# Optimization experiments

Hardware: AMD Instinct MI355X
Metric: run time of the kernel (lower is better)

Reference implementation:

```python
import jax, jax.numpy as jnp
import numpy as np

B, N, E, D = 8, 2048, 4096, 256
HOPS = 3

def setup_inputs() -> dict:
    key = jax.random.key(0)
    ks = jax.random.split(key, 12)
    p = lambda k, shp: (jax.random.normal(k, shp, dtype=jnp.float32) * 0.02)
    return {
        "node_vec": jax.random.normal(ks[0], (B, N, D), dtype=jnp.float32),
        "edge_vec": jax.random.normal(ks[1], (B, E, D), dtype=jnp.float32),
        "node2edge": jax.random.uniform(ks[2], (B, E, N), dtype=jnp.float32),
        "edge2node": jax.random.uniform(ks[3], (B, N, E), dtype=jnp.float32),
        "node_mask": jnp.ones((B, N), dtype=jnp.float32),
        "W_fuse": p(ks[4], (D, 2 * D)), "b_fuse": jnp.zeros((D,), jnp.float32),
        "W_z": p(ks[5], (D, 4 * D)), "b_z": jnp.zeros((D,), jnp.float32),
        "W_update": p(ks[6], (D, 2 * D)),
        "W_reset": p(ks[7], (D, 2 * D)),
        "W_memory": p(ks[8], (D, 2 * D)),
        "W_max": p(ks[9], (D, D)),
    }

def _gnn_step(node_vec, edge_vec, n2e, e2n, W_fuse, b_fuse):
    # n2e: [B,E,N], e2n: [B,N,E]
    edge_emb = jnp.einsum('ben,bnd->bed', n2e, node_vec)          # [B,E,D]
    edge_emb = jax.nn.relu(jnp.concatenate([edge_emb, edge_vec], axis=-1) @ W_fuse.T + b_fuse)
    norm = jnp.sum(e2n, axis=2, keepdims=True) + 1.0               # [B,N,1]
    return (jnp.einsum('bne,bed->bnd', e2n, edge_emb) + node_vec) / norm

def _gated_fusion(in_vec, out_vec, W_z, b_z):
    feats = jnp.concatenate([in_vec, out_vec, in_vec * out_vec, in_vec - out_vec], axis=-1)
    z = jax.nn.sigmoid(feats @ W_z.T + b_z)
    return (1.0 - z) * in_vec + z * out_vec

def _gru_step(cur, new, W_u, W_r, W_m):
    cn = jnp.concatenate([cur, new], axis=-1)
    u = jax.nn.sigmoid(cn @ W_u.T)
    r = jax.nn.sigmoid(cn @ W_r.T)
    m = jnp.tanh(jnp.concatenate([r * cur, new], axis=-1) @ W_m.T)
    return (1.0 - u) * cur + u * m

def reference(node_vec, edge_vec, node2edge, edge2node, node_mask,
              W_fuse, b_fuse, W_z, b_z, W_update, W_reset, W_memory, W_max):
    n2e_T = jnp.swapaxes(node2edge, 1, 2)  # [B,N,E]
    e2n_T = jnp.swapaxes(edge2node, 1, 2)  # [B,E,N]
    for _ in range(HOPS):
        out_vec = _gnn_step(node_vec, edge_vec, node2edge, edge2node, W_fuse, b_fuse)
        in_vec = _gnn_step(node_vec, edge_vec, e2n_T, n2e_T, W_fuse, b_fuse)
        new_vec = _gated_fusion(in_vec, out_vec, W_z, b_z)
        node_vec = _gru_step(node_vec, new_vec, W_update, W_reset, W_memory)
    # graph max-pooling: linear then max over nodes (node_mask unused, as in original)
    graph_embedding = jnp.max(node_vec @ W_max.T, axis=1)          # [B,D]
    return (jnp.swapaxes(node_vec, 0, 1), graph_embedding[None])    # [N,B,D], [1,B,D]
```

## Files before the change

kernel.cpp:

```cpp
#include <hip/hip_runtime.h>
#include <math.h>

#define Bb 8
#define Nn 2048
#define Ee 4096
#define Dd 256
#define HOPS 3

typedef __attribute__((ext_vector_type(4))) float f32x4;
typedef _Float16 f16;
typedef __attribute__((ext_vector_type(8))) _Float16 f16x8;
typedef __attribute__((ext_vector_type(4))) _Float16 f16x4;
typedef __attribute__((ext_vector_type(8))) short s16x8;
typedef __attribute__((ext_vector_type(4))) short s16x4;

__device__ __forceinline__ short f2bf(float f){
  union{float f; unsigned u;} x; x.f=f;
  unsigned r = (x.u + 0x7fffu + ((x.u>>16)&1u)) >> 16;
  return (short)r;
}
__device__ __forceinline__ float bf2f(short h){
  union{unsigned u; float f;} x; x.u = ((unsigned)(unsigned short)h) << 16; return x.f;
}
__device__ __forceinline__ int swz(int row, int idx){ return idx ^ ((row & 7) << 3); }

enum { HN=0, HT=1 };
enum { OF=0, OH=1, OHT=2 };
enum { EP_NONE=0, EP_BIAS, EP_ADDRELU, EP_AGG };
enum { SM_CN=0, SM_G4, SM_RC };
enum { SE_GATE=0, SE_SIG, SE_TANH };

template<int AMODE, bool AH, int SPL, int EPI, int OUTM>
__global__ __launch_bounds__(512) void hgemm(
    const void* __restrict__ Av, const f16* __restrict__ Bh, void* __restrict__ Cv,
    const float* __restrict__ aux1, const float* __restrict__ aux2,
    const float* __restrict__ bias,
    int M, int Nd, int K, int lda, int ldb, int ldc,
    long sA, long sB, long sC, long sAux1, long sAux2,
    long aLo, long bLo, int maskB, int mask1)
{
  const int bz = blockIdx.z;
  const char* Ab = (const char*)Av + (AH ? bz * sA * 2 : bz * sA * 4);
  Bh += (long)(bz & maskB) * sB;
  char* Cb = (char*)Cv + ((OUTM == OF) ? bz * sC * 4 : bz * sC * 2);
  if (aux1) aux1 += (long)(bz & mask1) * sAux1;
  if (aux2) aux2 += bz * sAux2;
  const int m0 = blockIdx.y * 128;
  const int n0 = blockIdx.x * 128;

  constexpr int HLA = 128 * 64;
  constexpr int HLB = 128 * 64;
  __shared__ f16 As[128 * 64 * ((SPL & 2) ? 2 : 1)];
  __shared__ f16 Bs[128 * 64 * ((SPL & 1) ? 2 : 1)];

  const int tid = threadIdx.x;
  const int wid = tid >> 6, lane = tid & 63;
  const int wm = (wid >> 1) * 32, wn = (wid & 1) * 64;
  const int r = lane & 15, g = lane >> 4;

  f32x4 acc[2][4];
  #pragma unroll
  for (int i = 0; i < 2; i++)
    #pragma unroll
    for (int j = 0; j < 4; j++) acc[i][j] = (f32x4){0.f, 0.f, 0.f, 0.f};

  f16x8 ra0, ra1, rl0, rl1;
  f16x8 rb0, rb1, rbl0, rbl1;

  auto loadA = [&](int k0) {
    if (AMODE == HN && AH) {
      const f16* Ah = (const f16*)Ab;
      const int row = tid >> 2, kc = (tid & 3) * 16;
      const long off = (long)(m0 + row) * lda + k0 + kc;
      ra0 = *(const f16x8*)&Ah[off];
      ra1 = *(const f16x8*)&Ah[off + 8];
      if (SPL & 2) { rl0 = *(const f16x8*)&Ah[aLo + off]; rl1 = *(const f16x8*)&Ah[aLo + off + 8]; }
    } else if (AMODE == HN && !AH) {
      const float* Af = (const float*)Ab;
      const int row = tid >> 2, kc = (tid & 3) * 16;
      const float* s = &Af[(long)(m0 + row) * lda + k0 + kc];
      f32x4 v0 = *(const f32x4*)s,       v1 = *(const f32x4*)(s + 4);
      f32x4 v2 = *(const f32x4*)(s + 8), v3 = *(const f32x4*)(s + 12);
      ra0 = (f16x8){(f16)v0.x,(f16)v0.y,(f16)v0.z,(f16)v0.w,(f16)v1.x,(f16)v1.y,(f16)v1.z,(f16)v1.w};
      ra1 = (f16x8){(f16)v2.x,(f16)v2.y,(f16)v2.z,(f16)v2.w,(f16)v3.x,(f16)v3.y,(f16)v3.z,(f16)v3.w};
    } else {
      const int mm = tid & 127, kh = (tid >> 7) * 16;
      if (AH) {
        const f16* s = &((const f16*)Ab)[(long)(k0 + kh) * lda + m0 + mm];
        #pragma unroll
        for (int j = 0; j < 8; j++) ra0[j] = s[(long)j * lda];
        #pragma unroll
        for (int j = 0; j < 8; j++) ra1[j] = s[(long)(j + 8) * lda];
      } else {
        const float* s = &((const float*)Ab)[(long)(k0 + kh) * lda + m0 + mm];
        #pragma unroll
        for (int j = 0; j < 8; j++) ra0[j] = (f16)s[(long)j * lda];
        #pragma unroll
        for (int j = 0; j < 8; j++) ra1[j] = (f16)s[(long)(j + 8) * lda];
      }
    }
  };
  auto storeA = [&]() {
    if (AMODE == HT) {
      const int mm = tid & 127, kh = (tid >> 7) * 16;
      *(f16x8*)&As[swz(mm, mm * 64 + kh)]     = ra0;
      *(f16x8*)&As[swz(mm, mm * 64 + kh + 8)] = ra1;
    } else {
      const int row = tid >> 2, kc = (tid & 3) * 16;
      const int i0 = swz(row, row * 64 + kc), i1 = swz(row, row * 64 + kc + 8);
      *(f16x8*)&As[i0] = ra0;
      *(f16x8*)&As[i1] = ra1;
      if (SPL & 2) { *(f16x8*)&As[HLA + i0] = rl0; *(f16x8*)&As[HLA + i1] = rl1; }
    }
  };
  auto loadB = [&](int k0) {
    const int row = tid >> 2, kc = (tid & 3) * 16;
    const long off = (long)(n0 + row) * ldb + k0 + kc;
    rb0 = *(const f16x8*)&Bh[off];
    rb1 = *(const f16x8*)&Bh[off + 8];
    if (SPL & 1) { rbl0 = *(const f16x8*)&Bh[bLo + off]; rbl1 = *(const f16x8*)&Bh[bLo + off + 8]; }
  };
  auto storeB = [&]() {
    const int row = tid >> 2, kc = (tid & 3) * 16;
    const int i0 = swz(row, row * 64 + kc), i1 = swz(row, row * 64 + kc + 8);
    *(f16x8*)&Bs[i0] = rb0;
    *(f16x8*)&Bs[i1] = rb1;
    if (SPL & 1) { *(f16x8*)&Bs[HLB + i0] = rbl0; *(f16x8*)&Bs[HLB + i1] = rbl1; }
  };

  loadA(0); loadB(0);
  storeA(); storeB();
  __syncthreads();

  const int NT = K >> 6;
  for (int t = 0; t < NT; t++) {
    const bool more = (t + 1 < NT);
    if (more) { loadA((t + 1) << 6); loadB((t + 1) << 6); }
    #pragma unroll
    for (int ks = 0; ks < 2; ks++) {
      f16x8 af[2], bf[4], afl[2], bfl[4];
      #pragma unroll
      for (int i = 0; i < 2; i++) {
        const int rw = wm + i * 16 + r;
        const int ix = swz(rw, rw * 64 + ks * 32 + g * 8);
        af[i] = *(const f16x8*)&As[ix];
        if (SPL & 2) afl[i] = *(const f16x8*)&As[HLA + ix];
      }
      #pragma unroll
      for (int j = 0; j < 4; j++) {
        const int rw = wn + j * 16 + r;
        const int ix = swz(rw, rw * 64 + ks * 32 + g * 8);
        bf[j] = *(const f16x8*)&Bs[ix];
        if (SPL & 1) bfl[j] = *(const f16x8*)&Bs[HLB + ix];
      }
      #pragma unroll
      for (int i = 0; i < 2; i++)
        #pragma unroll
        for (int j = 0; j < 4; j++) {
          acc[i][j] = __builtin_amdgcn_mfma_f32_16x16x32_f16(af[i], bf[j], acc[i][j], 0, 0, 0);
          if (SPL & 1)
            acc[i][j] = __builtin_amdgcn_mfma_f32_16x16x32_f16(af[i], bfl[j], acc[i][j], 0, 0, 0);
          if (SPL & 2)
            acc[i][j] = __builtin_amdgcn_mfma_f32_16x16x32_f16(afl[i], bf[j], acc[i][j], 0, 0, 0);
        }
    }
    __syncthreads();
    if (more) { storeA(); storeB(); __syncthreads(); }
  }

  if (OUTM == OHT) {
    f16* tile = (f16*)Bs;
    #pragma unroll
    for (int half = 0; half < 2; half++) {
      __syncthreads();
      if ((wm >> 6) == half) {
        #pragma unroll
        for (int i = 0; i < 2; i++)
          #pragma unroll
          for (int j = 0; j < 4; j++) {
            const int rowl = wm + i * 16 + g * 4 - 64 * half;
            const int coll = wn + j * 16 + r;
            #pragma unroll
            for (int t = 0; t < 4; t++) {
              float v = acc[i][j][t];
              if (EPI == EP_ADDRELU) {
                v += aux1[(long)(m0 + 64 * half + rowl + t) * 256 + n0 + coll];
                v = v > 0.f ? v : 0.f;
              } else if (EPI == EP_BIAS) { v += bias[n0 + coll]; }
              tile[coll * 72 + rowl + t] = (f16)v;
            }
          }
      }
      __syncthreads();
      const int c2 = tid >> 2, rs = (tid & 3) * 16;
      f16* dst = &((f16*)Cb)[(long)(n0 + c2) * ldc + m0 + 64 * half + rs];
      *(f16x8*)dst       = *(const f16x8*)&tile[c2 * 72 + rs];
      *(f16x8*)(dst + 8) = *(const f16x8*)&tile[c2 * 72 + rs + 8];
    }
  } else {
    #pragma unroll
    for (int i = 0; i < 2; i++) {
      #pragma unroll
      for (int j = 0; j < 4; j++) {
        const int rowb = m0 + wm + i * 16 + g * 4;
        const int col = n0 + wn + j * 16 + r;
        #pragma unroll
        for (int t = 0; t < 4; t++) {
          const int row = rowb + t;
          const long idx = (long)row * ldc + col;
          float v = acc[i][j][t];
          if (EPI == EP_BIAS)         { v += bias[col]; }
          else if (EPI == EP_ADDRELU) { v += aux1[(long)row * 256 + col]; v = v > 0.f ? v : 0.f; }
          else if (EPI == EP_AGG)     { v = (v + aux1[idx]) * aux2[row]; }
          if (OUTM == OH) ((f16*)Cb)[idx] = (f16)v;
          else            ((float*)Cb)[idx] = v;
        }
      }
    }
  }
}

template<int AMODE, int EPI>
__global__ __launch_bounds__(512) void ggemm(
    const float* __restrict__ A, const float* __restrict__ A2, const float* __restrict__ A3,
    const short* __restrict__ Bw, float* __restrict__ C,
    const float* __restrict__ aux1, const float* __restrict__ aux2, const float* __restrict__ bias,
    int Nd, int K, int lda, int ldb, int ldc, long bLo)
{
  const int m0 = blockIdx.y * 128;
  const int n0 = blockIdx.x * 128;
  constexpr int HLA = 128 * 64;
  constexpr int HLB = 128 * 64;
  __shared__ short As[128 * 64 * 2];
  __shared__ short Bs[128 * 64 * 2];

  const int tid = threadIdx.x;
  const int wid = tid >> 6, lane = tid & 63;
  const int wm = (wid >> 1) * 32, wn = (wid & 1) * 64;
  const int r = lane & 15, g = lane >> 4;

  f32x4 acc[2][4];
  #pragma unroll
  for (int i = 0; i < 2; i++)
    #pragma unroll
    for (int j = 0; j < 4; j++) acc[i][j] = (f32x4){0.f, 0.f, 0.f, 0.f};

  s16x4 rah[4], ral[4];
  s16x8 rbh0, rbh1, rbl0, rbl1;

  auto loadA = [&](int k0) {
    const int row = tid >> 2, kc = (tid & 3) * 16;
    const int kk = k0 + kc, q = kk >> 8, kd = kk & 255;
    const long base = (long)(m0 + row) * 256 + kd;
    const long baseA = (long)(m0 + row) * lda + kd;
    #pragma unroll
    for (int u = 0; u < 4; u++) {
      f32x4 v;
      if (AMODE == SM_CN) {
        v = (q == 0) ? *(const f32x4*)(A + base + 4 * u)
                     : *(const f32x4*)(A2 + base + 4 * u);
      } else if (AMODE == SM_G4) {
        if (q == 0)      v = *(const f32x4*)(A  + base + 4 * u);
        else if (q == 1) v = *(const f32x4*)(A2 + base + 4 * u);
        else {
          f32x4 x = *(const f32x4*)(A  + base + 4 * u);
          f32x4 y = *(const f32x4*)(A2 + base + 4 * u);
          v = (q == 2) ? x * y : x - y;
        }
      } else {
        if (q == 0) {
          f32x4 x = *(const f32x4*)(A  + baseA + 4 * u);
          f32x4 y = *(const f32x4*)(A2 + base + 4 * u);
          v = x * y;
        } else v = *(const f32x4*)(A3 + base + 4 * u);
      }
      s16x4 h = { f2bf(v.x), f2bf(v.y), f2bf(v.z), f2bf(v.w) };
      rah[u] = h;
      ral[u] = (s16x4){ f2bf(v.x - bf2f(h.x)), f2bf(v.y - bf2f(h.y)),
                        f2bf(v.z - bf2f(h.z)), f2bf(v.w - bf2f(h.w)) };
    }
  };
  auto storeA = [&]() {
    const int row = tid >> 2, kc = (tid & 3) * 16;
    const int i0 = swz(row, row * 64 + kc), i1 = swz(row, row * 64 + kc + 8);
    *(s16x4*)&As[i0]     = rah[0]; *(s16x4*)&As[i0 + 4] = rah[1];
    *(s16x4*)&As[i1]     = rah[2]; *(s16x4*)&As[i1 + 4] = rah[3];
    *(s16x4*)&As[HLA + i0]     = ral[0]; *(s16x4*)&As[HLA + i0 + 4] = ral[1];
    *(s16x4*)&As[HLA + i1]     = ral[2]; *(s16x4*)&As[HLA + i1 + 4] = ral[3];
  };
  auto loadB = [&](int k0) {
    const int row = tid >> 2, kc = (tid & 3) * 16;
    const long off = (long)(n0 + row) * ldb + k0 + kc;
    rbh0 = *(const s16x8*)&Bw[off];
    rbh1 = *(const s16x8*)&Bw[off + 8];
    rbl0 = *(const s16x8*)&Bw[bLo + off];
    rbl1 = *(const s16x8*)&Bw[bLo + off + 8];
  };
  auto storeB = [&]() {
    const int row = tid >> 2, kc = (tid & 3) * 16;
    const int i0 = swz(row, row * 64 + kc), i1 = swz(row, row * 64 + kc + 8);
    *(s16x8*)&Bs[i0] = rbh0;
    *(s16x8*)&Bs[i1] = rbh1;
    *(s16x8*)&Bs[HLB + i0] = rbl0;
    *(s16x8*)&Bs[HLB + i1] = rbl1;
  };

  loadA(0); loadB(0);
  storeA(); storeB();
  __syncthreads();

  const int NT = K >> 6;
  for (int t = 0; t < NT; t++) {
    const bool more = (t + 1 < NT);
    if (more) { loadA((t + 1) << 6); loadB((t + 1) << 6); }
    #pragma unroll
    for (int ks = 0; ks < 2; ks++) {
      s16x8 ah[2], al[2], bh[4], bl[4];
      #pragma unroll
      for (int i = 0; i < 2; i++) {
        const int rw = wm + i * 16 + r;
        const int ix = swz(rw, rw * 64 + ks * 32 + g * 8);
        ah[i] = *(const s16x8*)&As[ix];
        al[i] = *(const s16x8*)&As[HLA + ix];
      }
      #pragma unroll
      for (int j = 0; j < 4; j++) {
        const int rw = wn + j * 16 + r;
        const int ix = swz(rw, rw * 64 + ks * 32 + g * 8);
        bh[j] = *(const s16x8*)&Bs[ix];
        bl[j] = *(const s16x8*)&Bs[HLB + ix];
      }
      #pragma unroll
      for (int i = 0; i < 2; i++)
        #pragma unroll
        for (int j = 0; j < 4; j++) {
          acc[i][j] = __builtin_amdgcn_mfma_f32_16x16x32_bf16(ah[i], bh[j], acc[i][j], 0, 0, 0);
          acc[i][j] = __builtin_amdgcn_mfma_f32_16x16x32_bf16(ah[i], bl[j], acc[i][j], 0, 0, 0);
          acc[i][j] = __builtin_amdgcn_mfma_f32_16x16x32_bf16(al[i], bh[j], acc[i][j], 0, 0, 0);
        }
    }
    __syncthreads();
    if (more) { storeA(); storeB(); __syncthreads(); }
  }

  #pragma unroll
  for (int i = 0; i < 2; i++) {
    #pragma unroll
    for (int j = 0; j < 4; j++) {
      #pragma unroll
      for (int t = 0; t < 4; t++) {
        const int row = m0 + wm + i * 16 + g * 4 + t;
        const int col = n0 + wn + j * 16 + r;
        float v = acc[i][j][t];
        if (EPI == SE_GATE) {
          v += bias[col];
          float z = 1.f / (1.f + __expf(-v));
          const long ix = (long)row * 256 + col;
          v = (1.f - z) * aux1[ix] + z * aux2[ix];
        } else if (EPI == SE_SIG) {
          v = 1.f / (1.f + __expf(-v));
        } else {
          v = tanhf(v);
        }
        C[(long)row * ldc + col] = v;
      }
    }
  }
}


__global__ void cvt_n2e_colsum(const float* __restrict__ n2e, f16* __restrict__ n2e_h,
                               float* __restrict__ part) {
  const int n = blockIdx.x * 256 + threadIdx.x;
  const int c = blockIdx.y, b = blockIdx.z;
  const long base = (long)b * Ee * Nn + (long)c * 256 * Nn + n;
  float s = 0.f;
  for (int e = 0; e < 256; e++) {
    float v = n2e[base + (long)e * Nn];
    n2e_h[base + (long)e * Nn] = (f16)v;
    s += v;
  }
  part[((long)b * 16 + c) * Nn + n] = s;
}

__global__ void cvt_e2n_rowsum(const float* __restrict__ e2n, f16* __restrict__ e2n_h,
                               float* __restrict__ rno) {
  const long row = blockIdx.x;
  const int tid = threadIdx.x, lane = tid & 63, wid = tid >> 6;
  const float* p = e2n + row * Ee;
  f16* ph = e2n_h + row * Ee;
  float s = 0.f;
  for (int e = tid; e < Ee; e += 256) { float v = p[e]; ph[e] = (f16)v; s += v; }
  #pragma unroll
  for (int off = 32; off; off >>= 1) s += __shfl_down(s, off);
  __shared__ float wsum[4];
  if (lane == 0) wsum[wid] = s;
  __syncthreads();
  if (tid == 0) rno[row] = 1.f / (1.f + wsum[0] + wsum[1] + wsum[2] + wsum[3]);
}

__global__ void adjT(const f16* __restrict__ in, f16* __restrict__ out, int R, int C) {
  __shared__ f16 t[64][72];
  const long boff = (long)blockIdx.z * R * C;
  const int r0 = blockIdx.x * 64, c0 = blockIdx.y * 64;
  const int tid = threadIdx.x;
  const int rl = tid >> 2, cl = (tid & 3) * 16;
  const f16* src = in + boff + (long)(r0 + rl) * C + c0 + cl;
  *(f16x8*)&t[rl][cl]     = *(const f16x8*)src;
  *(f16x8*)&t[rl][cl + 8] = *(const f16x8*)(src + 8);
  __syncthreads();
  const int cl2 = tid >> 2, rl2 = (tid & 3) * 16;
  f16x8 o0, o1;
  #pragma unroll
  for (int v = 0; v < 8; v++) { o0[v] = t[rl2 + v][cl2]; o1[v] = t[rl2 + 8 + v][cl2]; }
  f16* dst = out + boff + (long)(c0 + cl2) * R + r0 + rl2;
  *(f16x8*)dst = o0;
  *(f16x8*)(dst + 8) = o1;
}

__global__ void rowsum_kernel(const float* __restrict__ e2n, float* __restrict__ out) {
  const int gw = blockIdx.x * 4 + (threadIdx.x >> 6);
  const int lane = threadIdx.x & 63;
  const float* p = e2n + (long)gw * Ee;
  float s = 0.f;
  for (int e = lane; e < Ee; e += 64) s += p[e];
  #pragma unroll
  for (int off = 32; off; off >>= 1) s += __shfl_down(s, off);
  if (lane == 0) out[gw] = 1.f / (1.f + s);
}
__global__ void colsum_kernel(const float* __restrict__ n2e, float* __restrict__ part) {
  const int n = blockIdx.x * 256 + threadIdx.x;
  const int c = blockIdx.y, b = blockIdx.z;
  const float* p = n2e + (long)b * Ee * Nn + (long)c * 256 * Nn + n;
  float s = 0.f;
  for (int e = 0; e < 256; e++) s += p[(long)e * Nn];
  part[((long)b * 16 + c) * Nn + n] = s;
}
__global__ void colfin_kernel(const float* __restrict__ part, float* __restrict__ rni) {
  const int i = blockIdx.x * 256 + threadIdx.x;
  const int b = i >> 11, n = i & 2047;
  float s = 0.f;
  #pragma unroll
  for (int c = 0; c < 16; c++) s += part[((long)b * 16 + c) * Nn + n];
  rni[i] = 1.f / (1.f + s);
}

__global__ void cvt_half(const float* __restrict__ src, f16* __restrict__ dst) {
  const long i4 = (long)blockIdx.x * 256 + threadIdx.x;
  f32x4 v = *(const f32x4*)&src[i4 * 4];
  *(f16x4*)&dst[i4 * 4] = (f16x4){(f16)v.x, (f16)v.y, (f16)v.z, (f16)v.w};
}

__global__ void cvt_half_split(const float* __restrict__ src, f16* __restrict__ dst, long loOff) {
  const long i4 = (long)blockIdx.x * 256 + threadIdx.x;
  f32x4 v = *(const f32x4*)&src[i4 * 4];
  f16x4 h = {(f16)v.x, (f16)v.y, (f16)v.z, (f16)v.w};
  *(f16x4*)&dst[i4 * 4] = h;
  f16x4 l = {(f16)(v.x - (float)h[0]), (f16)(v.y - (float)h[1]),
             (f16)(v.z - (float)h[2]), (f16)(v.w - (float)h[3])};
  *(f16x4*)&dst[loOff + i4 * 4] = l;
}

__global__ void cvt_bf_split(const float* __restrict__ src, short* __restrict__ dst, long loOff) {
  const long i4 = (long)blockIdx.x * 256 + threadIdx.x;
  f32x4 v = *(const f32x4*)&src[i4 * 4];
  s16x4 h = { f2bf(v.x), f2bf(v.y), f2bf(v.z), f2bf(v.w) };
  *(s16x4*)&dst[i4 * 4] = h;
  s16x4 l = { f2bf(v.x - bf2f(h.x)), f2bf(v.y - bf2f(h.y)),
              f2bf(v.z - bf2f(h.z)), f2bf(v.w - bf2f(h.w)) };
  *(s16x4*)&dst[loOff + i4 * 4] = l;
}

__global__ void init_cur(const float* __restrict__ node_vec, float* __restrict__ cur,
                         f16* __restrict__ cur_h, long loOff) {
  const long i4 = (long)blockIdx.x * 256 + threadIdx.x;
  f32x4 v = *(const f32x4*)&node_vec[i4 * 4];
  *(f32x4*)&cur[i4 * 4] = v;
  f16x4 h = {(f16)v.x, (f16)v.y, (f16)v.z, (f16)v.w};
  *(f16x4*)&cur_h[i4 * 4] = h;
  f16x4 l = {(f16)(v.x - (float)h[0]), (f16)(v.y - (float)h[1]),
             (f16)(v.z - (float)h[2]), (f16)(v.w - (float)h[3])};
  *(f16x4*)&cur_h[loOff + i4 * 4] = l;
}

__global__ void transposeT(const float* __restrict__ cur, f16* __restrict__ curT, long loOff) {
  __shared__ f16 th[64][72];
  __shared__ f16 tl[64][72];
  const int b = blockIdx.z, nt = blockIdx.x * 64, dt = blockIdx.y * 64;
  const int tid = threadIdx.x;
  const int nl = tid >> 2, d0 = (tid & 3) * 16;
  const float* src = cur + ((long)b * Nn + nt + nl) * 256 + dt + d0;
  #pragma unroll
  for (int u = 0; u < 4; u++) {
    f32x4 v = *(const f32x4*)(src + 4 * u);
    f16x4 h = {(f16)v.x, (f16)v.y, (f16)v.z, (f16)v.w};
    *(f16x4*)&th[nl][d0 + 4 * u] = h;
    f16x4 l = {(f16)(v.x - (float)h[0]), (f16)(v.y - (float)h[1]),
               (f16)(v.z - (float)h[2]), (f16)(v.w - (float)h[3])};
    *(f16x4*)&tl[nl][d0 + 4 * u] = l;
  }
  __syncthreads();
  const int dl = tid >> 2, n0l = (tid & 3) * 16;
  f16x8 o0, o1, p0, p1;
  #pragma unroll
  for (int v = 0; v < 8; v++) {
    o0[v] = th[n0l + v][dl];     o1[v] = th[n0l + 8 + v][dl];
    p0[v] = tl[n0l + v][dl];     p1[v] = tl[n0l + 8 + v][dl];
  }
  f16* dst = curT + (long)b * (256 * Nn) + (long)(dt + dl) * Nn + nt + n0l;
  *(f16x8*)dst = o0;
  *(f16x8*)(dst + 8) = o1;
  *(f16x8*)(dst + loOff) = p0;
  *(f16x8*)(dst + loOff + 8) = p1;
}

__global__ void gruf_kernel(const float* __restrict__ urb, const float* __restrict__ m,
                            float* __restrict__ cur, f16* __restrict__ cur_h, long loOff) {
  const long i = (long)blockIdx.x * 256 + threadIdx.x;
  const long bn = i >> 8; const int d = i & 255;
  const float uu = urb[bn * 512 + d];
  const float v = (1.f - uu) * cur[i] + uu * m[i];
  cur[i] = v;
  f16 h = (f16)v;
  cur_h[i] = h;
  cur_h[loOff + i] = (f16)(v - (float)h);
}

__global__ void maxpool1(const float* __restrict__ pooled, float* __restrict__ part) {
  const int d = threadIdx.x, c = blockIdx.x, b = blockIdx.y;
  const float* p = pooled + ((long)b * Nn + c * 256) * Dd + d;
  float m = -INFINITY;
  for (int n = 0; n < 256; n++) m = fmaxf(m, p[(long)n * Dd]);
  part[(b * 8 + c) * Dd + d] = m;
}
__global__ void maxpool2(const float* __restrict__ part, float* __restrict__ out1) {
  const int d = threadIdx.x, b = blockIdx.x;
  float m = -INFINITY;
  #pragma unroll
  for (int c = 0; c < 8; c++) m = fmaxf(m, part[(b * 8 + c) * Dd + d]);
  out1[b * Dd + d] = m;
}
__global__ void transpose_out(const float* __restrict__ cur, float* __restrict__ out0) {
  const long i = (long)blockIdx.x * 256 + threadIdx.x;
  const int d = i & 255;
  const long nb = i >> 8;
  const int b = nb & 7;
  const long n = nb >> 3;
  out0[i] = cur[((long)b * Nn + n) * Dd + d];
}

extern "C" void kernel_launch(void* const* d_in, const int* in_sizes, int n_in,
                              void* d_out, int out_size, void* d_ws, size_t ws_size,
                              hipStream_t stream) {
  const float* node_vec = (const float*)d_in[0];
  const float* edge_vec = (const float*)d_in[1];
  const float* n2e      = (const float*)d_in[2];
  const float* e2n      = (const float*)d_in[3];
  const float* W_fuse   = (const float*)d_in[5];
  const float* b_fuse   = (const float*)d_in[6];
  const float* W_z      = (const float*)d_in[7];
  const float* b_z      = (const float*)d_in[8];
  const float* W_u      = (const float*)d_in[9];
  const float* W_r      = (const float*)d_in[10];
  const float* W_m      = (const float*)d_in[11];
  const float* W_max    = (const float*)d_in[12];

  const long ND  = (long)Bb * Nn * Dd;
  const long EDb = (long)Ee * Dd;
  const long NDb = (long)Nn * Dd;
  const long ED  = (long)Bb * EDb;
  const long ADJb = (long)Ee * Nn;
  const long ADJ = (long)Bb * ADJb;
  const int  BN  = Bb * Nn;

  char* p = (char*)d_ws;
  auto alloc = [&](size_t bytes) { char* r = p; p += (bytes + 255) & ~(size_t)255; return r; };

  const size_t need_full =
      (size_t)4 * ADJ * 2
      + (size_t)ED * 2
      + (size_t)4 * ED * 2
      + (size_t)ED * 4
      + (size_t)4 * ND * 2
      + (size_t)(2 * 131072 + 2 * 65536) * 2
      + (size_t)(2 * 262144 + 2 * 262144 + 2 * 131072) * 2
      + (size_t)5 * ND * 4
      + (size_t)BN * 512 * 4
      + (size_t)(2 * BN + 16 * BN + BN) * 4
      + 64 * 1024;
  const bool full = ws_size >= need_full;

  f16 *adjEO = nullptr, *adjAG = nullptr;
  f16 *n2e_h = nullptr, *e2n_hT = nullptr, *e2n_h = nullptr, *n2e_hT = nullptr;
  if (full) {
    adjEO = (f16*)alloc((size_t)2 * ADJ * 2);
    adjAG = (f16*)alloc((size_t)2 * ADJ * 2);
    n2e_h = adjEO;  e2n_hT = adjEO + ADJ;
    e2n_h = adjAG;  n2e_hT = adjAG + ADJ;
  }
  f16* ev_h    = (f16*)alloc(ED * 2);
  f16* E1h2    = (f16*)alloc((size_t)2 * ED * 2);
  f16* E2T2    = (f16*)alloc((size_t)2 * ED * 2);
  float* EVW   = (float*)alloc(ED * 4);
  f16* cur_h   = (f16*)alloc(2 * ND * 2);
  f16* cur_hT  = (f16*)alloc(2 * ND * 2);
  f16* Wf_h    = (f16*)alloc(2 * 131072 * 2);
  f16* Wmax_h  = (f16*)alloc(2 * 65536 * 2);
  short* Wz_s  = (short*)alloc((size_t)2 * 262144 * 2);
  short* Wur_s = (short*)alloc((size_t)2 * 262144 * 2);
  short* Wm_s  = (short*)alloc((size_t)2 * 131072 * 2);
  float* cur   = (float*)alloc(ND * 4);
  float* outv  = (float*)alloc(2 * ND * 4);
  float* inv   = outv + ND;
  float* nv    = (float*)alloc(ND * 4);
  float* urb   = (float*)alloc((size_t)BN * 512 * 4);
  float* mb    = (float*)alloc(ND * 4);
  float* rno   = (float*)alloc(2 * BN * 4);
  float* rni   = rno + BN;
  float* colpart = (float*)alloc((size_t)16 * BN * 4);
  float* maxpart = (float*)alloc(BN * 4);

  float* out0 = (float*)d_out;
  float* out1 = out0 + ND;

  if (full) {
    cvt_n2e_colsum<<<dim3(Nn / 256, 16, Bb), 256, 0, stream>>>(n2e, n2e_h, colpart);
    colfin_kernel<<<BN / 256, 256, 0, stream>>>(colpart, rni);
    cvt_e2n_rowsum<<<BN, 256, 0, stream>>>(e2n, e2n_h, rno);
    adjT<<<dim3(Ee / 64, Nn / 64, Bb), 256, 0, stream>>>(n2e_h, n2e_hT, Ee, Nn);
    adjT<<<dim3(Nn / 64, Ee / 64, Bb), 256, 0, stream>>>(e2n_h, e2n_hT, Nn, Ee);
  } else {
    colsum_kernel<<<dim3(Nn / 256, 16, Bb), 256, 0, stream>>>(n2e, colpart);
    colfin_kernel<<<BN / 256, 256, 0, stream>>>(colpart, rni);
    rowsum_kernel<<<BN / 4, 256, 0, stream>>>(e2n, rno);
  }
  cvt_half<<<(int)(ED / 1024), 256, 0, stream>>>(edge_vec, ev_h);
  cvt_half_split<<<131072 / 1024, 256, 0, stream>>>(W_fuse, Wf_h, 131072);
  cvt_half_split<<<65536 / 1024, 256, 0, stream>>>(W_max, Wmax_h, 65536);
  cvt_bf_split<<<262144 / 1024, 256, 0, stream>>>(W_z, Wz_s, 262144);
  cvt_bf_split<<<131072 / 1024, 256, 0, stream>>>(W_u, Wur_s, 262144);
  cvt_bf_split<<<131072 / 1024, 256, 0, stream>>>(W_r, Wur_s + 131072, 262144);
  cvt_bf_split<<<131072 / 1024, 256, 0, stream>>>(W_m, Wm_s, 131072);
  init_cur<<<(int)(ND / 1024), 256, 0, stream>>>(node_vec, cur, cur_h, ND);
  transposeT<<<dim3(Nn / 64, 4, Bb), 256, 0, stream>>>(cur, cur_hT, ND);

  hgemm<HN, true, 1, EP_BIAS, OF><<<dim3(2, Ee / 128, Bb), 512, 0, stream>>>(
      ev_h, Wf_h + 256, EVW, nullptr, nullptr, b_fuse,
      Ee, 256, 256, 256, 512, 256, EDb, 0, EDb, 0, 0, 0, 131072, 0, 0);

  for (int h = 0; h < HOPS; h++) {
    if (full) {
      hgemm<HN, true, 1, EP_NONE, OH><<<dim3(2, Ee / 128, 2 * Bb), 512, 0, stream>>>(
          adjEO, cur_hT, E1h2, nullptr, nullptr, nullptr,
          Ee, 256, Nn, Nn, Nn, 256, ADJb, NDb, EDb, 0, 0, 0, ND, 7, 0);
      hgemm<HN, true, 1, EP_ADDRELU, OHT><<<dim3(2, Ee / 128, 2 * Bb), 512, 0, stream>>>(
          E1h2, Wf_h, E2T2, EVW, nullptr, nullptr,
          Ee, 256, 256, 256, 512, Ee, EDb, 0, EDb, EDb, 0, 0, 131072, 0, 7);
      hgemm<HN, true, 0, EP_AGG, OF><<<dim3(2, Nn / 128, 2 * Bb), 512, 0, stream>>>(
          adjAG, E2T2, outv, cur, rno, nullptr,
          Nn, 256, Ee, Ee, Ee, 256, ADJb, EDb, NDb, NDb, (long)Nn, 0, 0, 15, 7);
    } else {
      hgemm<HN, false, 1, EP_NONE, OH><<<dim3(2, Ee / 128, Bb), 512, 0, stream>>>(
          n2e, cur_hT, E1h2, nullptr, nullptr, nullptr,
          Ee, 256, Nn, Nn, Nn, 256, ADJb, NDb, EDb, 0, 0, 0, ND, 7, 0);
      hgemm<HT, false, 1, EP_NONE, OH><<<dim3(2, Ee / 128, Bb), 512, 0, stream>>>(
          e2n, cur_hT, E1h2 + ED, nullptr, nullptr, nullptr,
          Ee, 256, Nn, Ee, Nn, 256, ADJb, NDb, EDb, 0, 0, 0, ND, 7, 0);
      hgemm<HN, true, 1, EP_ADDRELU, OHT><<<dim3(2, Ee / 128, 2 * Bb), 512, 0, stream>>>(
          E1h2, Wf_h, E2T2, EVW, nullptr, nullptr,
          Ee, 256, 256, 256, 512, Ee, EDb, 0, EDb, EDb, 0, 0, 131072, 0, 7);
      hgemm<HN, false, 0, EP_AGG, OF><<<dim3(2, Nn / 128, Bb), 512, 0, stream>>>(
          e2n, E2T2, outv, cur, rno, nullptr,
          Nn, 256, Ee, Ee, Ee, 256, (long)Nn * Ee, EDb, NDb, NDb, (long)Nn, 0, 0, 15, 7);
      hgemm<HT, false, 0, EP_AGG, OF><<<dim3(2, Nn / 128, Bb), 512, 0, stream>>>(
          n2e, E2T2 + ED, inv, cur, rni, nullptr,
          Nn, 256, Ee, Nn, Ee, 256, (long)Ee * Nn, EDb, NDb, NDb, (long)Nn, 0, 0, 15, 7);
    }
    ggemm<SM_G4, SE_GATE><<<dim3(2, BN / 128, 1), 512, 0, stream>>>(
        inv, outv, nullptr, Wz_s, nv, inv, outv, b_z, 256, 1024, 256, 1024, 256, 262144);
    ggemm<SM_CN, SE_SIG><<<dim3(4, BN / 128, 1), 512, 0, stream>>>(
        cur, nv, nullptr, Wur_s, urb, nullptr, nullptr, nullptr, 512, 512, 256, 512, 512, 262144);
    ggemm<SM_RC, SE_TANH><<<dim3(2, BN / 128, 1), 512, 0, stream>>>(
        urb + 256, cur, nv, Wm_s, mb, nullptr, nullptr, nullptr, 256, 512, 512, 512, 256, 131072);
    gruf_kernel<<<(int)(ND / 256), 256, 0, stream>>>(urb, mb, cur, cur_h, ND);
    if (h < HOPS - 1)
      transposeT<<<dim3(Nn / 64, 4, Bb), 256, 0, stream>>>(cur, cur_hT, ND);
  }

  hgemm<HN, true, 3, EP_NONE, OF><<<dim3(2, BN / 128, 1), 512, 0, stream>>>(
      cur_h, Wmax_h, urb, nullptr, nullptr, nullptr,
      BN, 256, 256, 256, 256, 256, 0, 0, 0, 0, 0, ND, 65536, 0, 0);
  maxpool1<<<dim3(8, Bb), 256, 0, stream>>>(urb, maxpart);
  maxpool2<<<Bb, 256, 0, stream>>>(maxpart, out1);

  transpose_out<<<(int)(ND / 256), 256, 0, stream>>>(cur, out0);
}
```

Baseline: 1.709 ms.

## Fuse adjacency fp16 conversion, transpose and sums; store edge projection in fp16

The two-pass preprocessing (convert-plus-sum kernels followed by separate transpose kernels) is replaced by one cvt_dual kernel per adjacency. It reads the fp32 matrix once and writes both the fp16 copy and its transpose, along with partial row or column sums that a small finalize kernel reduces. This removes a full re-read of the fp16 adjacencies. The precomputed edge_vec projection is also stored in fp16 and read as fp16 in the ReLU epilogue, halving that auxiliary traffic at some cost in precision. The sums for the transposed case are now taken from fp16-rounded values.

```diff
diff --git a/kernel.cpp b/kernel.cpp
--- a/kernel.cpp
+++ b/kernel.cpp
@@ -26,7 +26,7 @@
 
 enum { HN=0, HT=1 };
 enum { OF=0, OH=1, OHT=2 };
-enum { EP_NONE=0, EP_BIAS, EP_ADDRELU, EP_AGG };
+enum { EP_NONE=0, EP_BIAS, EP_ADDRELUH, EP_AGG };
 enum { SM_CN=0, SM_G4, SM_RC };
 enum { SE_GATE=0, SE_SIG, SE_TANH };
 
@@ -183,8 +183,8 @@
             #pragma unroll
             for (int t = 0; t < 4; t++) {
               float v = acc[i][j][t];
-              if (EPI == EP_ADDRELU) {
-                v += aux1[(long)(m0 + 64 * half + rowl + t) * 256 + n0 + coll];
+              if (EPI == EP_ADDRELUH) {
+                v += (float)((const f16*)aux1)[(long)(m0 + 64 * half + rowl + t) * 256 + n0 + coll];
                 v = v > 0.f ? v : 0.f;
               } else if (EPI == EP_BIAS) { v += bias[n0 + coll]; }
               tile[coll * 72 + rowl + t] = (f16)v;
@@ -209,9 +209,10 @@
           const int row = rowb + t;
           const long idx = (long)row * ldc + col;
           float v = acc[i][j][t];
-          if (EPI == EP_BIAS)         { v += bias[col]; }
-          else if (EPI == EP_ADDRELU) { v += aux1[(long)row * 256 + col]; v = v > 0.f ? v : 0.f; }
-          else if (EPI == EP_AGG)     { v = (v + aux1[idx]) * aux2[row]; }
+          if (EPI == EP_BIAS)          { v += bias[col]; }
+          else if (EPI == EP_ADDRELUH) { v += (float)((const f16*)aux1)[(long)row * 256 + col];
+                                         v = v > 0.f ? v : 0.f; }
+          else if (EPI == EP_AGG)      { v = (v + aux1[idx]) * aux2[row]; }
           if (OUTM == OH) ((f16*)Cb)[idx] = (f16)v;
           else            ((float*)Cb)[idx] = v;
         }
@@ -369,53 +370,59 @@
 }
 
 
-__global__ void cvt_n2e_colsum(const float* __restrict__ n2e, f16* __restrict__ n2e_h,
-                               float* __restrict__ part) {
-  const int n = blockIdx.x * 256 + threadIdx.x;
-  const int c = blockIdx.y, b = blockIdx.z;
-  const long base = (long)b * Ee * Nn + (long)c * 256 * Nn + n;
-  float s = 0.f;
-  for (int e = 0; e < 256; e++) {
-    float v = n2e[base + (long)e * Nn];
-    n2e_h[base + (long)e * Nn] = (f16)v;
-    s += v;
-  }
-  part[((long)b * 16 + c) * Nn + n] = s;
-}
-
-__global__ void cvt_e2n_rowsum(const float* __restrict__ e2n, f16* __restrict__ e2n_h,
-                               float* __restrict__ rno) {
-  const long row = blockIdx.x;
-  const int tid = threadIdx.x, lane = tid & 63, wid = tid >> 6;
-  const float* p = e2n + row * Ee;
-  f16* ph = e2n_h + row * Ee;
-  float s = 0.f;
-  for (int e = tid; e < Ee; e += 256) { float v = p[e]; ph[e] = (f16)v; s += v; }
-  #pragma unroll
-  for (int off = 32; off; off >>= 1) s += __shfl_down(s, off);
-  __shared__ float wsum[4];
-  if (lane == 0) wsum[wid] = s;
-  __syncthreads();
-  if (tid == 0) rno[row] = 1.f / (1.f + wsum[0] + wsum[1] + wsum[2] + wsum[3]);
-}
-
-__global__ void adjT(const f16* __restrict__ in, f16* __restrict__ out, int R, int C) {
+template<bool SUMDST>
+__global__ void cvt_dual(const float* __restrict__ in, f16* __restrict__ outR,
+                         f16* __restrict__ outT, float* __restrict__ part, int R, int C) {
   __shared__ f16 t[64][72];
-  const long boff = (long)blockIdx.z * R * C;
+  __shared__ float sacc[64][4];
+  const long boff = (long)blockIdx.z * (long)R * C;
   const int r0 = blockIdx.x * 64, c0 = blockIdx.y * 64;
   const int tid = threadIdx.x;
   const int rl = tid >> 2, cl = (tid & 3) * 16;
-  const f16* src = in + boff + (long)(r0 + rl) * C + c0 + cl;
-  *(f16x8*)&t[rl][cl]     = *(const f16x8*)src;
-  *(f16x8*)&t[rl][cl + 8] = *(const f16x8*)(src + 8);
+  const float* src = in + boff + (long)(r0 + rl) * C + c0 + cl;
+  f16 loc[16];
+  float s = 0.f;
+  #pragma unroll
+  for (int u = 0; u < 4; u++) {
+    f32x4 v = *(const f32x4*)(src + 4 * u);
+    loc[4*u+0] = (f16)v.x; loc[4*u+1] = (f16)v.y; loc[4*u+2] = (f16)v.z; loc[4*u+3] = (f16)v.w;
+    if (!SUMDST) s += v.x + v.y + v.z + v.w;
+  }
+  f16* dR = outR + boff + (long)(r0 + rl) * C + c0 + cl;
+  *(f16x8*)dR       = *(const f16x8*)&loc[0];
+  *(f16x8*)(dR + 8) = *(const f16x8*)&loc[8];
+  *(f16x8*)&t[rl][cl]     = *(const f16x8*)&loc[0];
+  *(f16x8*)&t[rl][cl + 8] = *(const f16x8*)&loc[8];
+  if (!SUMDST) sacc[rl][tid & 3] = s;
   __syncthreads();
   const int cl2 = tid >> 2, rl2 = (tid & 3) * 16;
   f16x8 o0, o1;
   #pragma unroll
   for (int v = 0; v < 8; v++) { o0[v] = t[rl2 + v][cl2]; o1[v] = t[rl2 + 8 + v][cl2]; }
-  f16* dst = out + boff + (long)(c0 + cl2) * R + r0 + rl2;
-  *(f16x8*)dst = o0;
-  *(f16x8*)(dst + 8) = o1;
+  if (SUMDST) {
+    float s2 = 0.f;
+    #pragma unroll
+    for (int v = 0; v < 8; v++) s2 += (float)o0[v] + (float)o1[v];
+    sacc[cl2][tid & 3] = s2;
+  }
+  f16* dT = outT + boff + (long)(c0 + cl2) * R + r0 + rl2;
+  *(f16x8*)dT = o0;
+  *(f16x8*)(dT + 8) = o1;
+  __syncthreads();
+  if (tid < 64) {
+    float tot = sacc[tid][0] + sacc[tid][1] + sacc[tid][2] + sacc[tid][3];
+    const int slot = SUMDST ? blockIdx.x : blockIdx.y;
+    const int n    = (SUMDST ? c0 : r0) + tid;
+    part[((long)blockIdx.z * 64 + slot) * Nn + n] = tot;
+  }
+}
+
+__global__ void colfin64(const float* __restrict__ part, float* __restrict__ rn) {
+  const int i = blockIdx.x * 256 + threadIdx.x;
+  const int b = i >> 11, n = i & 2047;
+  float s = 0.f;
+  for (int c = 0; c < 64; c++) s += part[((long)b * 64 + c) * Nn + n];
+  rn[i] = 1.f / (1.f + s);
 }
 
 __global__ void rowsum_kernel(const float* __restrict__ e2n, float* __restrict__ out) {
@@ -436,7 +443,7 @@
   for (int e = 0; e < 256; e++) s += p[(long)e * Nn];
   part[((long)b * 16 + c) * Nn + n] = s;
 }
-__global__ void colfin_kernel(const float* __restrict__ part, float* __restrict__ rni) {
+__global__ void colfin16(const float* __restrict__ part, float* __restrict__ rni) {
   const int i = blockIdx.x * 256 + threadIdx.x;
   const int b = i >> 11, n = i & 2047;
   float s = 0.f;
@@ -580,13 +587,13 @@
       (size_t)4 * ADJ * 2
       + (size_t)ED * 2
       + (size_t)4 * ED * 2
-      + (size_t)ED * 4
+      + (size_t)ED * 2
       + (size_t)4 * ND * 2
       + (size_t)(2 * 131072 + 2 * 65536) * 2
       + (size_t)(2 * 262144 + 2 * 262144 + 2 * 131072) * 2
       + (size_t)5 * ND * 4
       + (size_t)BN * 512 * 4
-      + (size_t)(2 * BN + 16 * BN + BN) * 4
+      + (size_t)(2 * BN + 2 * 64 * BN) * 4
       + 64 * 1024;
   const bool full = ws_size >= need_full;
 
@@ -601,7 +608,7 @@
   f16* ev_h    = (f16*)alloc(ED * 2);
   f16* E1h2    = (f16*)alloc((size_t)2 * ED * 2);
   f16* E2T2    = (f16*)alloc((size_t)2 * ED * 2);
-  float* EVW   = (float*)alloc(ED * 4);
+  f16* EVWh    = (f16*)alloc(ED * 2);
   f16* cur_h   = (f16*)alloc(2 * ND * 2);
   f16* cur_hT  = (f16*)alloc(2 * ND * 2);
   f16* Wf_h    = (f16*)alloc(2 * 131072 * 2);
@@ -617,21 +624,23 @@
   float* mb    = (float*)alloc(ND * 4);
   float* rno   = (float*)alloc(2 * BN * 4);
   float* rni   = rno + BN;
-  float* colpart = (float*)alloc((size_t)16 * BN * 4);
+  float* rnopart = (float*)alloc((size_t)64 * BN * 4);
+  float* rnipart = (float*)alloc((size_t)64 * BN * 4);
   float* maxpart = (float*)alloc(BN * 4);
 
   float* out0 = (float*)d_out;
   float* out1 = out0 + ND;
 
   if (full) {
-    cvt_n2e_colsum<<<dim3(Nn / 256, 16, Bb), 256, 0, stream>>>(n2e, n2e_h, colpart);
-    colfin_kernel<<<BN / 256, 256, 0, stream>>>(colpart, rni);
-    cvt_e2n_rowsum<<<BN, 256, 0, stream>>>(e2n, e2n_h, rno);
-    adjT<<<dim3(Ee / 64, Nn / 64, Bb), 256, 0, stream>>>(n2e_h, n2e_hT, Ee, Nn);
-    adjT<<<dim3(Nn / 64, Ee / 64, Bb), 256, 0, stream>>>(e2n_h, e2n_hT, Nn, Ee);
+    cvt_dual<false><<<dim3(Nn / 64, Ee / 64, Bb), 256, 0, stream>>>(
+        e2n, e2n_h, e2n_hT, rnopart, Nn, Ee);
+    cvt_dual<true><<<dim3(Ee / 64, Nn / 64, Bb), 256, 0, stream>>>(
+        n2e, n2e_h, n2e_hT, rnipart, Ee, Nn);
+    colfin64<<<BN / 256, 256, 0, stream>>>(rnopart, rno);
+    colfin64<<<BN / 256, 256, 0, stream>>>(rnipart, rni);
   } else {
-    colsum_kernel<<<dim3(Nn / 256, 16, Bb), 256, 0, stream>>>(n2e, colpart);
-    colfin_kernel<<<BN / 256, 256, 0, stream>>>(colpart, rni);
+    colsum_kernel<<<dim3(Nn / 256, 16, Bb), 256, 0, stream>>>(n2e, rnipart);
+    colfin16<<<BN / 256, 256, 0, stream>>>(rnipart, rni);
     rowsum_kernel<<<BN / 4, 256, 0, stream>>>(e2n, rno);
   }
   cvt_half<<<(int)(ED / 1024), 256, 0, stream>>>(edge_vec, ev_h);
@@ -644,8 +653,8 @@
   init_cur<<<(int)(ND / 1024), 256, 0, stream>>>(node_vec, cur, cur_h, ND);
   transposeT<<<dim3(Nn / 64, 4, Bb), 256, 0, stream>>>(cur, cur_hT, ND);
 
-  hgemm<HN, true, 1, EP_BIAS, OF><<<dim3(2, Ee / 128, Bb), 512, 0, stream>>>(
-      ev_h, Wf_h + 256, EVW, nullptr, nullptr, b_fuse,
+  hgemm<HN, true, 1, EP_BIAS, OH><<<dim3(2, Ee / 128, Bb), 512, 0, stream>>>(
+      ev_h, Wf_h + 256, EVWh, nullptr, nullptr, b_fuse,
       Ee, 256, 256, 256, 512, 256, EDb, 0, EDb, 0, 0, 0, 131072, 0, 0);
 
   for (int h = 0; h < HOPS; h++) {
@@ -653,9 +662,9 @@
       hgemm<HN, true, 1, EP_NONE, OH><<<dim3(2, Ee / 128, 2 * Bb), 512, 0, stream>>>(
           adjEO, cur_hT, E1h2, nullptr, nullptr, nullptr,
           Ee, 256, Nn, Nn, Nn, 256, ADJb, NDb, EDb, 0, 0, 0, ND, 7, 0);
-      hgemm<HN, true, 1, EP_ADDRELU, OHT><<<dim3(2, Ee / 128, 2 * Bb), 512, 0, stream>>>(
-          E1h2, Wf_h, E2T2, EVW, nullptr, nullptr,
-          Ee, 256, 256, 256, 512, Ee, EDb, 0, EDb, EDb, 0, 0, 131072, 0, 7);
+      hgemm<HN, true, 1, EP_ADDRELUH, OHT><<<dim3(2, Ee / 128, 2 * Bb), 512, 0, stream>>>(
+          E1h2, Wf_h, E2T2, (const float*)EVWh, nullptr, nullptr,
+          Ee, 256, 256, 256, 512, Ee, EDb, 0, EDb, EDb / 2, 0, 0, 131072, 0, 7);
       hgemm<HN, true, 0, EP_AGG, OF><<<dim3(2, Nn / 128, 2 * Bb), 512, 0, stream>>>(
           adjAG, E2T2, outv, cur, rno, nullptr,
           Nn, 256, Ee, Ee, Ee, 256, ADJb, EDb, NDb, NDb, (long)Nn, 0, 0, 15, 7);
@@ -666,9 +675,9 @@
       hgemm<HT, false, 1, EP_NONE, OH><<<dim3(2, Ee / 128, Bb), 512, 0, stream>>>(
           e2n, cur_hT, E1h2 + ED, nullptr, nullptr, nullptr,
           Ee, 256, Nn, Ee, Nn, 256, ADJb, NDb, EDb, 0, 0, 0, ND, 7, 0);
-      hgemm<HN, true, 1, EP_ADDRELU, OHT><<<dim3(2, Ee / 128, 2 * Bb), 512, 0, stream>>>(
-          E1h2, Wf_h, E2T2, EVW, nullptr, nullptr,
-          Ee, 256, 256, 256, 512, Ee, EDb, 0, EDb, EDb, 0, 0, 131072, 0, 7);
+      hgemm<HN, true, 1, EP_ADDRELUH, OHT><<<dim3(2, Ee / 128, 2 * Bb), 512, 0, stream>>>(
+          E1h2, Wf_h, E2T2, (const float*)EVWh, nullptr, nullptr,
+          Ee, 256, 256, 256, 512, Ee, EDb, 0, EDb, EDb / 2, 0, 0, 131072, 0, 7);
       hgemm<HN, false, 0, EP_AGG, OF><<<dim3(2, Nn / 128, Bb), 512, 0, stream>>>(
           e2n, E2T2, outv, cur, rno, nullptr,
           Nn, 256, Ee, Ee, Ee, 256, (long)Nn * Ee, EDb, NDb, NDb, (long)Nn, 0, 0, 15, 7);
```

New measurement: 1.665 ms. 1.03x faster.
